# Kernel tuning notes

Hardware: AMD Instinct MI355X
Metric: run time of the kernel (lower is better)

The kernel has to match this reference:

```python
import jax, jax.numpy as jnp
import numpy as np

TOKENS, D_IN, D_OUT, N_FACTORS, RANK = 8192, 4096, 4096, 2, 64


def setup_inputs() -> dict:
    key = jax.random.key(0)
    ks = jax.random.split(key, 6)
    # kaiming_uniform-ish scales (exact init distribution is irrelevant for correctness)
    w_bound = 1.0 / np.sqrt(D_IN)
    x = jax.random.normal(ks[0], (TOKENS, D_IN), dtype=jnp.float32)
    W = jax.random.uniform(ks[1], (D_OUT, D_IN), jnp.float32, -w_bound, w_bound)
    bias = jax.random.uniform(ks[2], (D_OUT,), jnp.float32, -w_bound, w_bound)
    a_bound = 1.0 / np.sqrt(RANK)
    As = jax.random.uniform(ks[3], (N_FACTORS, D_OUT, RANK), jnp.float32, -a_bound, a_bound)
    Bs = jax.random.normal(ks[4], (N_FACTORS, RANK, RANK), dtype=jnp.float32) * 0.1
    # Cs initialized nonzero here so the low-rank path actually contributes
    Cs = jax.random.normal(ks[5], (N_FACTORS, RANK, D_IN), dtype=jnp.float32) * 0.02
    return {"x": x, "W": W, "bias": bias, "As": As, "Bs": Bs, "Cs": Cs}


def reference(x, W, bias, As, Bs, Cs):
    # W_eff = W + sum_f tanh(A_f) @ B_f @ C_f   (phi_A = tanh, B already transformed)
    # [f,o,r] x [f,r,k] -> [f,o,k]; then x [f,k,i] -> [o,i] summed over f
    AB = jnp.einsum('for,frk->fok', jnp.tanh(As), Bs)
    W_eff = W + jnp.einsum('fok,fki->oi', AB, Cs)
    # F.linear: x @ W_eff^T + bias
    return jnp.einsum('ti,oi->to', x, W_eff) + bias
```

## Files before the change

kernel.cpp:

```cpp
#include <hip/hip_runtime.h>
#include <hip/hip_bf16.h>

typedef __bf16 bf16x8 __attribute__((ext_vector_type(8)));
typedef float f32x4 __attribute__((ext_vector_type(4)));

#define TOKENS 8192
#define D_IN   4096
#define D_OUT  4096

static __device__ __forceinline__ unsigned short f2bf(float f) {
  union { float f; unsigned int u; } v; v.f = f;
  unsigned int r = v.u + 0x7FFFu + ((v.u >> 16) & 1u);
  return (unsigned short)(r >> 16);
}

__global__ void prep_kernel(const float* __restrict__ x,
                            unsigned short* __restrict__ xb,
                            const float* __restrict__ Cs,
                            unsigned short* __restrict__ Cst,
                            const float* __restrict__ As,
                            const float* __restrict__ Bs,
                            unsigned short* __restrict__ ABt) {
  __shared__ float shbuf[4352];
  const int t = threadIdx.x;
  if (blockIdx.x < 16384) {
    size_t i = ((size_t)blockIdx.x * 256 + t) * 8;
    float4 a = *(const float4*)(x + i);
    float4 b = *(const float4*)(x + i + 4);
    union { unsigned short h[8]; uint4 u; } p;
    p.h[0] = f2bf(a.x); p.h[1] = f2bf(a.y);
    p.h[2] = f2bf(a.z); p.h[3] = f2bf(a.w);
    p.h[4] = f2bf(b.x); p.h[5] = f2bf(b.y);
    p.h[6] = f2bf(b.z); p.h[7] = f2bf(b.w);
    *(uint4*)(xb + i) = p.u;
  } else if (blockIdx.x < 16512) {
    float (*tp)[65] = (float(*)[65])shbuf;
    const int b2 = blockIdx.x - 16384;
    const int k0 = (b2 & 1) * 64;
    const int i0 = (b2 >> 1) * 64;
#pragma unroll
    for (int j = 0; j < 16; ++j) {
      int e = t + 256 * j;
      tp[e >> 6][e & 63] = Cs[(size_t)(k0 + (e >> 6)) * 4096 + i0 + (e & 63)];
    }
    __syncthreads();
#pragma unroll
    for (int j = 0; j < 16; ++j) {
      int e = t + 256 * j;
      Cst[(size_t)(i0 + (e >> 6)) * 128 + k0 + (e & 63)] =
          f2bf(tp[e & 63][e >> 6]);
    }
  } else {
    float (*tA)[64] = (float(*)[64])shbuf;
    float (*sB)[64] = (float(*)[64])(shbuf + 256);
    const int ab = blockIdx.x - 16512;
    const int f = ab >> 10;
    const int o0 = (ab & 1023) * 4;
    const int ol = t >> 6;
    const int k  = t & 63;
    tA[ol][k] = tanhf(As[((size_t)f * 4096 + o0 + ol) * 64 + k]);
#pragma unroll
    for (int j = 0; j < 16; ++j) {
      int e = t + 256 * j;
      sB[e >> 6][e & 63] = Bs[f * 4096 + e];
    }
    __syncthreads();
    float acc = 0.f;
#pragma unroll
    for (int r = 0; r < 64; ++r) acc += tA[ol][r] * sB[r][k];
    ABt[(size_t)(o0 + ol) * 128 + f * 64 + k] = f2bf(acc);
  }
}

__global__ __launch_bounds__(256) void weff_kernel(
    const float* __restrict__ W,
    const unsigned short* __restrict__ ABt,
    const unsigned short* __restrict__ Cst,
    unsigned short* __restrict__ Weff) {
  const int KW = 128;
  __shared__ __align__(16) unsigned short sA[128 * 64];
  __shared__ __align__(16) unsigned short sB[128 * 64];
  const int t = threadIdx.x;
  const int lane = t & 63;
  const int wave = t >> 6;
  const int bi = blockIdx.x, bo = blockIdx.y;
  const int wm = (wave & 1) * 64, wn = (wave >> 1) * 64;

  const int tr = t >> 3;
  const int cg = (t & 7) ^ (tr & 7);
  const unsigned short* agA = ABt + (size_t)(bo * 128 + tr) * KW + cg * 8;
  const unsigned short* agB = Cst + (size_t)(bi * 128 + tr) * KW + cg * 8;
  unsigned short* const la = sA + t * 8;
  unsigned short* const lb = sB + t * 8;

  f32x4 acc[4][4] = {};
  const int lm = lane & 15;
  const int cb = lane >> 4;
  const int sw = lm & 7;

  for (int kt = 0; kt < KW; kt += 64) {
    __syncthreads();
#pragma unroll
    for (int j = 0; j < 4; ++j) {
      __builtin_amdgcn_global_load_lds(
          (const __attribute__((address_space(1))) void*)(agA + (size_t)j * 32 * KW + kt),
          (__attribute__((address_space(3))) void*)(la + j * 2048), 16, 0, 0);
      __builtin_amdgcn_global_load_lds(
          (const __attribute__((address_space(1))) void*)(agB + (size_t)j * 32 * KW + kt),
          (__attribute__((address_space(3))) void*)(lb + j * 2048), 16, 0, 0);
    }
    __syncthreads();
#pragma unroll
    for (int ks = 0; ks < 2; ++ks) {
      const int ch = ((ks * 4 + cb) ^ sw) * 8;
      bf16x8 af[4], bfr[4];
#pragma unroll
      for (int mi = 0; mi < 4; ++mi)
        af[mi] = *(const bf16x8*)(sA + (wm + mi * 16 + lm) * 64 + ch);
#pragma unroll
      for (int ni = 0; ni < 4; ++ni)
        bfr[ni] = *(const bf16x8*)(sB + (wn + ni * 16 + lm) * 64 + ch);
#pragma unroll
      for (int mi = 0; mi < 4; ++mi)
#pragma unroll
        for (int ni = 0; ni < 4; ++ni)
          acc[mi][ni] = __builtin_amdgcn_mfma_f32_16x16x32_bf16(
              af[mi], bfr[ni], acc[mi][ni], 0, 0, 0);
    }
  }

  const int cn = lane & 15;
  const int rm = (lane >> 4) * 4;
#pragma unroll
  for (int ni = 0; ni < 4; ++ni) {
    const int col = bi * 128 + wn + ni * 16 + cn;
#pragma unroll
    for (int mi = 0; mi < 4; ++mi) {
      const int row0 = bo * 128 + wm + mi * 16 + rm;
#pragma unroll
      for (int r = 0; r < 4; ++r) {
        const int row = row0 + r;
        Weff[(size_t)row * D_IN + col] =
            f2bf(W[(size_t)row * D_IN + col] + acc[mi][ni][r]);
      }
    }
  }
}


#define FENCE()   asm volatile("" ::: "memory")
#define BARRIER() do { FENCE(); __builtin_amdgcn_s_barrier(); FENCE(); } while (0)
#define WAITVM(n)  asm volatile("s_waitcnt vmcnt(" #n ")" ::: "memory")
#define SCHEDB()   __builtin_amdgcn_sched_barrier(0)
#define PRIO1      __builtin_amdgcn_s_setprio(1)
#define PRIO0      __builtin_amdgcn_s_setprio(0)

#define GLOAD(gptr, lptr)                                                     \
  __builtin_amdgcn_global_load_lds(                                           \
      (const __attribute__((address_space(1))) void*)(gptr),                  \
      (__attribute__((address_space(3))) void*)(lptr), 16, 0, 0)

#define STAGE_A(buf, h, kt) do {                                              \
    GLOAD(ag + (size_t)((h) * 128) * K + (kt),                                \
          lA + (buf) * 16384 + (h) * 8192);                                   \
    GLOAD(ag + (size_t)((h) * 128 + 64) * K + (kt),                           \
          lA + (buf) * 16384 + (h) * 8192 + 4096);                            \
  } while (0)
#define STAGE_B(buf, h, kt) do {                                              \
    GLOAD(bg + (size_t)((h) * 128) * K + (kt),                                \
          lB + (buf) * 16384 + (h) * 8192);                                   \
    GLOAD(bg + (size_t)((h) * 128 + 64) * K + (kt),                           \
          lB + (buf) * 16384 + (h) * 8192 + 4096);                            \
  } while (0)

#define LDA(buf, mi, ks) \
  (*(const bf16x8*)(rA + (buf) * 16384 + (mi) * 1024 + ((ks) ? ch1 : ch0)))
#define LDB(buf, ni, ks) \
  (*(const bf16x8*)(rB + (buf) * 16384 + (ni) * 1024 + ((ks) ? ch1 : ch0)))

#define READ_A(R0, R1, R2, R3, buf, mi0) do {                                 \
    R0 = LDA(buf, (mi0), 0);                                                  \
    R2 = LDA(buf, (mi0) + 1, 0);                                              \
    R1 = LDA(buf, (mi0), 1);                                                  \
    R3 = LDA(buf, (mi0) + 1, 1);                                              \
  } while (0)
#define READ_BSET(Bp, buf) do {                                               \
    Bp##00 = LDB(buf, 0, 0); Bp##10 = LDB(buf, 1, 0);                         \
    Bp##20 = LDB(buf, 2, 0); Bp##30 = LDB(buf, 3, 0);                         \
    Bp##01 = LDB(buf, 0, 1); Bp##11 = LDB(buf, 1, 1);                         \
    Bp##21 = LDB(buf, 2, 1); Bp##31 = LDB(buf, 3, 1);                         \
  } while (0)

#define MFMA1(d, a, b) \
  (d) = __builtin_amdgcn_mfma_f32_16x16x32_bf16((a), (b), (d), 0, 0, 0)

#define PBSET pb00, pb10, pb20, pb30, pb01, pb11, pb21, pb31
#define QBSET qb00, qb10, qb20, qb30, qb01, qb11, qb21, qb31
#define QUAD(...) QUAD_I(__VA_ARGS__)
#define QUAD_I(q, A0, A1, A2, A3, B00, B10, B20, B30, B01, B11, B21, B31)     \
    MFMA1(acc[2*(q)  ][0], A0, B00);                                          \
    MFMA1(acc[2*(q)+1][0], A2, B00);                                          \
    MFMA1(acc[2*(q)  ][1], A0, B10);                                          \
    MFMA1(acc[2*(q)+1][1], A2, B10);                                          \
    MFMA1(acc[2*(q)  ][2], A0, B20);                                          \
    MFMA1(acc[2*(q)+1][2], A2, B20);                                          \
    MFMA1(acc[2*(q)  ][3], A0, B30);                                          \
    MFMA1(acc[2*(q)+1][3], A2, B30);                                          \
    MFMA1(acc[2*(q)  ][0], A1, B01);                                          \
    MFMA1(acc[2*(q)+1][0], A3, B01);                                          \
    MFMA1(acc[2*(q)  ][1], A1, B11);                                          \
    MFMA1(acc[2*(q)+1][1], A3, B11);                                          \
    MFMA1(acc[2*(q)  ][2], A1, B21);                                          \
    MFMA1(acc[2*(q)+1][2], A3, B21);                                          \
    MFMA1(acc[2*(q)  ][3], A1, B31);                                          \
    MFMA1(acc[2*(q)+1][3], A3, B31);

#define GEMM_BODY(S2, S3, kt)                                                 \
  {                                                                           \
                                \
    READ_A(qa0, qa1, qa2, qa3, 0, 2);                                         \
    STAGE_A(1, 0, (kt) + 64); STAGE_A(1, 1, (kt) + 64);                       \
    BARRIER(); SCHEDB();                                                      \
    PRIO1; QUAD(0, pa0, pa1, pa2, pa3, PBSET); PRIO0; SCHEDB();               \
    BARRIER();                                                                \
                                \
    READ_A(pa0, pa1, pa2, pa3, 0, 4);                                         \
    if (S2) { STAGE_B(0, 0, (kt) + 128); STAGE_B(0, 1, (kt) + 128); }         \
    BARRIER(); SCHEDB();                                                      \
    PRIO1; QUAD(1, qa0, qa1, qa2, qa3, PBSET); PRIO0; SCHEDB();               \
    BARRIER();                                                                \
                                \
    READ_A(qa0, qa1, qa2, qa3, 0, 6);                                         \
    BARRIER(); SCHEDB();                                                      \
    PRIO1; QUAD(2, pa0, pa1, pa2, pa3, PBSET); PRIO0; SCHEDB();               \
    if (S2) { WAITVM(4); } else { WAITVM(0); }                                \
    BARRIER();                                                                \
                  \
    READ_A(pa0, pa1, pa2, pa3, 1, 0);                                         \
    READ_BSET(qb, 1);                                                         \
    BARRIER(); SCHEDB();                                                      \
    PRIO1; QUAD(3, qa0, qa1, qa2, qa3, PBSET); PRIO0; SCHEDB();               \
    BARRIER();                                                                \
                            \
    READ_A(qa0, qa1, qa2, qa3, 1, 2);                                         \
    if (S2) { STAGE_A(0, 0, (kt) + 128); STAGE_A(0, 1, (kt) + 128); }         \
    BARRIER(); SCHEDB();                                                      \
    PRIO1; QUAD(0, pa0, pa1, pa2, pa3, QBSET); PRIO0; SCHEDB();               \
    BARRIER();                                                                \
                            \
    READ_A(pa0, pa1, pa2, pa3, 1, 4);                                         \
    if (S3) { STAGE_B(1, 0, (kt) + 192); STAGE_B(1, 1, (kt) + 192); }         \
    BARRIER(); SCHEDB();                                                      \
    PRIO1; QUAD(1, qa0, qa1, qa2, qa3, QBSET); PRIO0; SCHEDB();               \
    BARRIER();                                                                \
                            \
    READ_A(qa0, qa1, qa2, qa3, 1, 6);                                         \
    BARRIER(); SCHEDB();                                                      \
    PRIO1; QUAD(2, pa0, pa1, pa2, pa3, QBSET); PRIO0; SCHEDB();               \
    if (S3) { WAITVM(4); } else { WAITVM(0); }                                \
    BARRIER();                                                                \
                \
    if (S2) { READ_A(pa0, pa1, pa2, pa3, 0, 0); READ_BSET(pb, 0); }           \
    BARRIER(); SCHEDB();                                                      \
    PRIO1; QUAD(3, qa0, qa1, qa2, qa3, QBSET); PRIO0; SCHEDB();               \
    BARRIER();                                                                \
  }

__global__ __launch_bounds__(512, 2) void gemm_kernel(
    const unsigned short* __restrict__ Abf,
    const unsigned short* __restrict__ Bbf,
    const float* __restrict__ bias,
    float* __restrict__ C) {
  const int K = D_IN, N = D_OUT;
  __shared__ __align__(16) unsigned short sA[2 * 256 * 64];
  __shared__ __align__(16) unsigned short sB[2 * 256 * 64];
  const int t = threadIdx.x;
  const int lane = t & 63;
  const int wave = t >> 6;

  const int wgid = blockIdx.y * gridDim.x + blockIdx.x;
  const int swz = (wgid & 7) * 64 + (wgid >> 3);
  const int bn = swz & 15;
  const int bm = swz >> 4;

  const int wm = (wave >> 2) * 128;
  const int wn = (wave & 3) * 64;

  const int tr = t >> 3;
  const int cg = (t & 7) ^ (tr & 7);
  const unsigned short* ag = Abf + (size_t)(bm * 256 + tr) * K + cg * 8;
  const unsigned short* bg = Bbf + (size_t)(bn * 256 + tr) * K + cg * 8;
  unsigned short* const lA = sA + t * 8;
  unsigned short* const lB = sB + t * 8;

  const int lm = lane & 15;
  const int cb = lane >> 4;
  const int sw = lm & 7;
  const int ch0 = ((cb) ^ sw) * 8;
  const int ch1 = ((4 + cb) ^ sw) * 8;
  const unsigned short* rA = sA + (wm + lm) * 64;
  const unsigned short* rB = sB + (wn + lm) * 64;

  f32x4 acc[8][4] = {};
  bf16x8 pa0, pa1, pa2, pa3;
  bf16x8 qa0, qa1, qa2, qa3;
  bf16x8 PBSET;
  bf16x8 QBSET;

  STAGE_B(0, 0, 0); STAGE_B(0, 1, 0);
  STAGE_A(0, 0, 0); STAGE_A(0, 1, 0);
  STAGE_B(1, 0, 64); STAGE_B(1, 1, 64);
  WAITVM(4);
  BARRIER();
  READ_BSET(pb, 0);
  READ_A(pa0, pa1, pa2, pa3, 0, 0);

#pragma unroll 1
  for (int kt = 0; kt < K - 128; kt += 128) GEMM_BODY(1, 1, kt)
  GEMM_BODY(0, 0, K - 128)

  const int cn = lane & 15;
  const int rm = (lane >> 4) * 4;
#pragma unroll
  for (int ni = 0; ni < 4; ++ni) {
    const int col = bn * 256 + wn + ni * 16 + cn;
    const float bv = bias[col];
#pragma unroll
    for (int mi = 0; mi < 8; ++mi) {
      const int row0 = bm * 256 + wm + mi * 16 + rm;
#pragma unroll
      for (int r = 0; r < 4; ++r)
        C[(size_t)(row0 + r) * N + col] = acc[mi][ni][r] + bv;
    }
  }
}

extern "C" void kernel_launch(void* const* d_in, const int* in_sizes, int n_in,
                              void* d_out, int out_size, void* d_ws, size_t ws_size,
                              hipStream_t stream) {
  const float* x    = (const float*)d_in[0];
  const float* W    = (const float*)d_in[1];
  const float* bias = (const float*)d_in[2];
  const float* As   = (const float*)d_in[3];
  const float* Bs   = (const float*)d_in[4];
  const float* Cs   = (const float*)d_in[5];
  float* out = (float*)d_out;

  char* ws = (char*)d_ws;
  unsigned short* ABt  = (unsigned short*)ws;
  unsigned short* Cst  = (unsigned short*)(ws + (1u << 20));
  unsigned short* Weff = (unsigned short*)(ws + (2u << 20));
  unsigned short* xb   = (unsigned short*)(ws + (2u << 20) + (32u << 20));

  prep_kernel<<<18560, 256, 0, stream>>>(x, xb, Cs, Cst, As, Bs, ABt);
  weff_kernel<<<dim3(32, 32), 256, 0, stream>>>(W, ABt, Cst, Weff);
  gemm_kernel<<<dim3(16, 32), 512, 0, stream>>>(xb, Weff, bias, out);
}
```

Measured before the change: 560.5 us.

## Interleave LDS reads, MFMAs and global loads with sched_group_barrier in GEMM loop

Restructures the main GEMM loop so each phase interleaves its LDS fragment reads with MFMAs and the global-to-LDS stage loads, using sched_group_barrier patterns. This replaces the previous split of read, barrier, compute, barrier per phase, halving the barriers. Global staging is spread one half-tile per phase and the A buffer for the next step is prefetched one phase earlier, including an extra prologue stage. The goal is to hide LDS and global latency behind matrix math. The risk is LDS hazards from the reordered stage/wait points and heavier register pressure.

```diff
diff --git a/kernel.cpp b/kernel.cpp
--- a/kernel.cpp
+++ b/kernel.cpp
@@ -151,9 +151,14 @@
 #define FENCE()   asm volatile("" ::: "memory")
 #define BARRIER() do { FENCE(); __builtin_amdgcn_s_barrier(); FENCE(); } while (0)
 #define WAITVM(n)  asm volatile("s_waitcnt vmcnt(" #n ")" ::: "memory")
-#define SCHEDB()   __builtin_amdgcn_sched_barrier(0)
 #define PRIO1      __builtin_amdgcn_s_setprio(1)
 #define PRIO0      __builtin_amdgcn_s_setprio(0)
+
+#define SG(mask, n) __builtin_amdgcn_sched_group_barrier(mask, n, 0)
+#define SG_4R() do { SG(0x100,1); SG(0x8,4); SG(0x100,1); SG(0x8,4);          \
+                     SG(0x100,1); SG(0x8,4); SG(0x100,1); SG(0x8,4); } while (0)
+#define SG_12R() do { SG(0x100,3); SG(0x8,4); SG(0x100,3); SG(0x8,4);         \
+                      SG(0x100,3); SG(0x8,4); SG(0x100,3); SG(0x8,4); } while (0)
 
 #define GLOAD(gptr, lptr)                                                     \
   __builtin_amdgcn_global_load_lds(                                           \
@@ -217,53 +222,75 @@
 
 #define GEMM_BODY(S2, S3, kt)                                                 \
   {                                                                           \
-                                \
-    READ_A(qa0, qa1, qa2, qa3, 0, 2);                                         \
-    STAGE_A(1, 0, (kt) + 64); STAGE_A(1, 1, (kt) + 64);                       \
-    BARRIER(); SCHEDB();                                                      \
-    PRIO1; QUAD(0, pa0, pa1, pa2, pa3, PBSET); PRIO0; SCHEDB();               \
-    BARRIER();                                                                \
-                                \
-    READ_A(pa0, pa1, pa2, pa3, 0, 4);                                         \
-    if (S2) { STAGE_B(0, 0, (kt) + 128); STAGE_B(0, 1, (kt) + 128); }         \
-    BARRIER(); SCHEDB();                                                      \
-    PRIO1; QUAD(1, qa0, qa1, qa2, qa3, PBSET); PRIO0; SCHEDB();               \
-    BARRIER();                                                                \
-                                \
-    READ_A(qa0, qa1, qa2, qa3, 0, 6);                                         \
-    BARRIER(); SCHEDB();                                                      \
-    PRIO1; QUAD(2, pa0, pa1, pa2, pa3, PBSET); PRIO0; SCHEDB();               \
-    if (S2) { WAITVM(4); } else { WAITVM(0); }                                \
-    BARRIER();                                                                \
-                  \
-    READ_A(pa0, pa1, pa2, pa3, 1, 0);                                         \
-    READ_BSET(qb, 1);                                                         \
-    BARRIER(); SCHEDB();                                                      \
-    PRIO1; QUAD(3, qa0, qa1, qa2, qa3, PBSET); PRIO0; SCHEDB();               \
-    BARRIER();                                                                \
-                            \
-    READ_A(qa0, qa1, qa2, qa3, 1, 2);                                         \
-    if (S2) { STAGE_A(0, 0, (kt) + 128); STAGE_A(0, 1, (kt) + 128); }         \
-    BARRIER(); SCHEDB();                                                      \
-    PRIO1; QUAD(0, pa0, pa1, pa2, pa3, QBSET); PRIO0; SCHEDB();               \
-    BARRIER();                                                                \
-                            \
-    READ_A(pa0, pa1, pa2, pa3, 1, 4);                                         \
-    if (S3) { STAGE_B(1, 0, (kt) + 192); STAGE_B(1, 1, (kt) + 192); }         \
-    BARRIER(); SCHEDB();                                                      \
-    PRIO1; QUAD(1, qa0, qa1, qa2, qa3, QBSET); PRIO0; SCHEDB();               \
-    BARRIER();                                                                \
-                            \
-    READ_A(qa0, qa1, qa2, qa3, 1, 6);                                         \
-    BARRIER(); SCHEDB();                                                      \
-    PRIO1; QUAD(2, pa0, pa1, pa2, pa3, QBSET); PRIO0; SCHEDB();               \
-    if (S3) { WAITVM(4); } else { WAITVM(0); }                                \
-    BARRIER();                                                                \
-                \
-    if (S2) { READ_A(pa0, pa1, pa2, pa3, 0, 0); READ_BSET(pb, 0); }           \
-    BARRIER(); SCHEDB();                                                      \
-    PRIO1; QUAD(3, qa0, qa1, qa2, qa3, QBSET); PRIO0; SCHEDB();               \
-    BARRIER();                                                                \
+    {                                                                 \
+      PRIO1;                                                                  \
+      READ_A(qa0, qa1, qa2, qa3, 0, 2);                                       \
+      QUAD(0, pa0, pa1, pa2, pa3, PBSET);                                     \
+      if (S2) STAGE_B(0, 0, (kt) + 128);                                      \
+      SG_4R(); if (S2) SG(0x20, 2);                                           \
+      PRIO0; BARRIER();                                                       \
+    }                                                                         \
+    {                                                                 \
+      PRIO1;                                                                  \
+      READ_A(pa0, pa1, pa2, pa3, 0, 4);                                       \
+      QUAD(1, qa0, qa1, qa2, qa3, PBSET);                                     \
+      if (S2) STAGE_B(0, 1, (kt) + 128);                                      \
+      SG_4R(); if (S2) SG(0x20, 2);                                           \
+      PRIO0; BARRIER();                                                       \
+    }                                                                         \
+    {                                                   \
+      PRIO1;                                                                  \
+      READ_A(qa0, qa1, qa2, qa3, 0, 6);                                       \
+      QUAD(2, pa0, pa1, pa2, pa3, PBSET);                                     \
+      SG_4R();                                                                \
+      PRIO0;                                                                  \
+      if (S2) { WAITVM(4); } else { WAITVM(0); }                              \
+      BARRIER();                                                              \
+    }                                                                         \
+    {                                                                 \
+      PRIO1;                                                                  \
+      READ_A(pa0, pa1, pa2, pa3, 1, 0);                                       \
+      READ_BSET(qb, 1);                                                       \
+      QUAD(3, qa0, qa1, qa2, qa3, PBSET);                                     \
+      if (S2) STAGE_A(0, 0, (kt) + 128);                                      \
+      SG_12R(); if (S2) SG(0x20, 2);                                          \
+      PRIO0; BARRIER();                                                       \
+    }                                                                         \
+    {                                                                 \
+      PRIO1;                                                                  \
+      READ_A(qa0, qa1, qa2, qa3, 1, 2);                                       \
+      QUAD(0, pa0, pa1, pa2, pa3, QBSET);                                     \
+      if (S2) STAGE_A(0, 1, (kt) + 128);                                      \
+      SG_4R(); if (S2) SG(0x20, 2);                                           \
+      PRIO0; BARRIER();                                                       \
+    }                                                                         \
+    {                                                                 \
+      PRIO1;                                                                  \
+      READ_A(pa0, pa1, pa2, pa3, 1, 4);                                       \
+      QUAD(1, qa0, qa1, qa2, qa3, QBSET);                                     \
+      if (S3) STAGE_B(1, 0, (kt) + 192);                                      \
+      SG_4R(); if (S3) SG(0x20, 2);                                           \
+      PRIO0; BARRIER();                                                       \
+    }                                                                         \
+    {                                                   \
+      PRIO1;                                                                  \
+      READ_A(qa0, qa1, qa2, qa3, 1, 6);                                       \
+      QUAD(2, pa0, pa1, pa2, pa3, QBSET);                                     \
+      if (S3) STAGE_B(1, 1, (kt) + 192);                                      \
+      SG_4R(); if (S3) SG(0x20, 2);                                           \
+      PRIO0;                                                                  \
+      if (S2) { WAITVM(4); } else { WAITVM(0); }                              \
+      BARRIER();                                                              \
+    }                                                                         \
+    {                                                                 \
+      PRIO1;                                                                  \
+      if (S2) { READ_A(pa0, pa1, pa2, pa3, 0, 0); READ_BSET(pb, 0); }         \
+      QUAD(3, qa0, qa1, qa2, qa3, QBSET);                                     \
+      if (S3) { STAGE_A(1, 0, (kt) + 192); STAGE_A(1, 1, (kt) + 192); }       \
+      if (S2) { SG_12R(); } else { SG(0x8, 16); }                             \
+      if (S3) SG(0x20, 4);                                                    \
+      PRIO0; BARRIER();                                                       \
+    }                                                                         \
   }
 
 __global__ __launch_bounds__(512, 2) void gemm_kernel(
@@ -310,10 +337,12 @@
   STAGE_B(0, 0, 0); STAGE_B(0, 1, 0);
   STAGE_A(0, 0, 0); STAGE_A(0, 1, 0);
   STAGE_B(1, 0, 64); STAGE_B(1, 1, 64);
-  WAITVM(4);
+  STAGE_A(1, 0, 64); STAGE_A(1, 1, 64);
+  WAITVM(8);
   BARRIER();
   READ_BSET(pb, 0);
   READ_A(pa0, pa1, pa2, pa3, 0, 0);
+  BARRIER();
 
 #pragma unroll 1
   for (int kt = 0; kt < K - 128; kt += 128) GEMM_BODY(1, 1, kt)
```

After: 527.8 us. 1.06x faster.
